# Performance work log

Hardware: AMD Instinct MI355X
Metric: run time of the kernel (lower is better)

Reference implementation:

```python
import jax, jax.numpy as jnp
import numpy as np

DIM = 1024
N_HEAD = 32
N_GROUP = 8
HEAD_DIM = DIM // N_HEAD  # 32
KV_DIM = N_GROUP * HEAD_DIM  # 256
BS, SEQ = 2, 2048


def setup_inputs() -> dict:
    key = jax.random.key(0)
    k1, k2, k3, k4 = jax.random.split(key, 4)
    x = jax.random.normal(k1, (BS, SEQ, DIM), dtype=jnp.float32)
    # nn.Linear weights, scaled like torch default init (~1/sqrt(fan_in))
    s = 1.0 / np.sqrt(DIM)
    wq = jax.random.normal(k2, (DIM, DIM), dtype=jnp.float32) * s
    wk = jax.random.normal(k3, (KV_DIM, DIM), dtype=jnp.float32) * s
    wv = jax.random.normal(k4, (KV_DIM, DIM), dtype=jnp.float32) * s
    return {"x": x, "wq": wq, "wk": wk, "wv": wv}


def reference(x, wq, wk, wv):
    bs, seq, _ = x.shape
    hpg = N_HEAD // N_GROUP  # heads per group
    # projections (torch Linear: x @ W.T)
    q = (x @ wq.T).reshape(bs, seq, N_GROUP, hpg, HEAD_DIM)
    k = (x @ wk.T).reshape(bs, seq, N_GROUP, HEAD_DIM)
    v = (x @ wv.T).reshape(bs, seq, N_GROUP, HEAD_DIM)
    # grouped attention: each KV group is shared by hpg query heads
    # (identical math to the expand/reshape in the torch source, no KV duplication)
    # NOTE: original applies NO 1/sqrt(head_dim) scaling and no mask.
    scores = jnp.einsum('bqgmd,bkgd->bgmqk', q, k)  # [bs, G, hpg, seq, seq]
    probs = jax.nn.softmax(scores, axis=-1)
    out = jnp.einsum('bgmqk,bkgd->bqgmd', probs, v)  # [bs, seq, G, hpg, hd]
    return out.reshape(bs, seq, N_HEAD * HEAD_DIM)
```

## Files before the change

### kernel.cpp

```cpp
#include <hip/hip_runtime.h>
#include <hip/hip_bf16.h>

#define BS   2
#define SEQ  2048
#define DIM  1024
#define HD   32
#define G    8
#define HPG  4
#define KVD  256
#define NTOT (DIM + 2*KVD)
#define NT2  (SEQ / 256)

typedef __attribute__((ext_vector_type(8))) _Float16 f16x8;
typedef __attribute__((ext_vector_type(4))) float f32x4;

__device__ __forceinline__ unsigned short f2h(float f) {
    _Float16 h = (_Float16)f;
    return __builtin_bit_cast(unsigned short, h);
}

__device__ __forceinline__ float fexp2(float x) { return __builtin_amdgcn_exp2f(x); }

#define GLDS(src, dst) __builtin_amdgcn_global_load_lds( \
    (const __attribute__((address_space(1))) unsigned int*)(src), \
    (__attribute__((address_space(3))) unsigned int*)(dst), 16, 0, 0)

#define NX4 1048576
__global__ __launch_bounds__(256) void cvt_all(const float* __restrict__ x,
                                               const float* __restrict__ wq,
                                               const float* __restrict__ wk,
                                               const float* __restrict__ wv,
                                               unsigned short* __restrict__ xb,
                                               unsigned short* __restrict__ wb) {
    int i = blockIdx.x * 256 + threadIdx.x;
    const float* src;
    unsigned short* dstb;
    int off, dsto;
    if (i < NX4) {
        src = x; off = i; dstb = xb; dsto = i;
    } else {
        int j = i - NX4;
        dstb = wb; dsto = j;
        if (j < 262144)      { src = wq; off = j; }
        else if (j < 327680) { src = wk; off = j - 262144; }
        else                 { src = wv; off = j - 327680; }
    }
    float4 v = reinterpret_cast<const float4*>(src)[off];
    ushort4 o;
    o.x = f2h(v.x); o.y = f2h(v.y); o.z = f2h(v.z); o.w = f2h(v.w);
    reinterpret_cast<ushort4*>(dstb)[dsto] = o;
}

__global__ __launch_bounds__(256) void qkv_gemm(const unsigned short* __restrict__ xb,
                                                const unsigned short* __restrict__ wb,
                                                unsigned short* __restrict__ qb,
                                                unsigned short* __restrict__ kb,
                                                unsigned short* __restrict__ vtb) {
    __shared__ unsigned short As[2][128 * 64];
    __shared__ unsigned short Bs[2][64 * 64];

    int tid  = threadIdx.x;
    int lane = tid & 63;
    int w    = tid >> 6;
    int m0   = blockIdx.y * 128;
    int n0   = blockIdx.x * 64;
    int lr = lane & 15, lq = lane >> 4;
    int wr = w >> 1, wc = w & 1;

    int srow = tid >> 3;
    int sg   = (tid & 7) ^ (srow & 7);
    const unsigned short* srcA = xb + (size_t)(m0 + srow) * DIM + sg * 8;
    const unsigned short* srcB = wb + (size_t)(n0 + srow) * DIM + sg * 8;

    #define GSTAGE(kt, buf) do { \
        GLDS(srcA + (kt),            &As[buf][tid * 8]); \
        GLDS(srcA + (kt) + 32 * DIM, &As[buf][(tid + 256) * 8]); \
        GLDS(srcA + (kt) + 64 * DIM, &As[buf][(tid + 512) * 8]); \
        GLDS(srcA + (kt) + 96 * DIM, &As[buf][(tid + 768) * 8]); \
        GLDS(srcB + (kt),            &Bs[buf][tid * 8]); \
        GLDS(srcB + (kt) + 32 * DIM, &Bs[buf][(tid + 256) * 8]); \
    } while (0)

    GSTAGE(0, 0);

    f32x4 acc[4][2] = {};
    int swz = lr & 7;

    for (int i = 0; i < 16; i++) {
        asm volatile("s_waitcnt vmcnt(0)" ::: "memory");
        __builtin_amdgcn_s_barrier();
        if (i + 1 < 16) GSTAGE((i + 1) * 64, (i + 1) & 1);

        const unsigned short* Ac = &As[i & 1][0];
        const unsigned short* Bc = &Bs[i & 1][0];

        #pragma unroll
        for (int ks = 0; ks < 2; ks++) {
            int c = ks * 4 + lq;
            f16x8 a[4], bfr[2];
            #pragma unroll
            for (int mi = 0; mi < 4; mi++) {
                int row = wr * 64 + mi * 16 + lr;
                a[mi] = *reinterpret_cast<const f16x8*>(Ac + row * 64 + (c ^ swz) * 8);
            }
            #pragma unroll
            for (int nf = 0; nf < 2; nf++) {
                int row = wc * 32 + nf * 16 + lr;
                bfr[nf] = *reinterpret_cast<const f16x8*>(Bc + row * 64 + (c ^ swz) * 8);
            }
            #pragma unroll
            for (int mi = 0; mi < 4; mi++)
                #pragma unroll
                for (int nf = 0; nf < 2; nf++)
                    acc[mi][nf] = __builtin_amdgcn_mfma_f32_16x16x32_f16(a[mi], bfr[nf], acc[mi][nf], 0, 0, 0);
        }
    }

    #pragma unroll
    for (int mi = 0; mi < 4; mi++) {
        #pragma unroll
        for (int nf = 0; nf < 2; nf++) {
            int col = n0 + wc * 32 + nf * 16 + lr;
            #pragma unroll
            for (int r = 0; r < 4; r++) {
                int row = m0 + wr * 64 + mi * 16 + lq * 4 + r;
                unsigned short v = f2h(acc[mi][nf][r]);
                if (col < DIM) {
                    qb[row * DIM + col] = v;
                } else if (col < DIM + KVD) {
                    kb[row * KVD + (col - DIM)] = v;
                } else {
                    int b = row >> 11, s = row & 2047;
                    int ps = (s & ~31) + ((s >> 2) & 3) * 8 + ((s >> 4) & 1) * 4 + (s & 3);
                    vtb[(b * KVD + (col - DIM - KVD)) * SEQ + ps] = v;
                }
            }
        }
    }
    #undef GSTAGE
}

__global__ __launch_bounds__(512) void gqa_attn(const unsigned short* __restrict__ qb,
                                                const unsigned short* __restrict__ kb,
                                                const unsigned short* __restrict__ vtb,
                                                float* __restrict__ out) {
    __shared__ unsigned short Ks[2][256 * 32];
    __shared__ unsigned short Vs[2][32 * 256];

    int tid  = threadIdx.x;
    int lane = tid & 63;
    int w    = tid >> 6;
    int head = w & 3;
    int qs   = (w >> 2) * 32;
    int bi   = blockIdx.x;
    int p  = bi & 15;
    int b  = p >> 3;
    int g  = p & 7;
    int qt = bi >> 4;
    int q0 = qt * 64;
    int lr = lane & 15, lq = lane >> 4;

    const unsigned short* kbase = kb + b * SEQ * KVD + g * HD;
    const unsigned short* vbase = vtb + (b * KVD + g * HD) * SEQ;

    int kr = tid >> 2;
    int swzK = (tid & 3) ^ ((kr >> 1) & 3);
    const unsigned short* srcK = kbase + kr * KVD + swzK * 8;
    int vr = tid >> 5;
    int swzV = (tid & 31) ^ (vr & 7);
    const unsigned short* srcV = vbase + vr * SEQ + swzV * 8;

    #define STAGE(tile, buf) do { \
        GLDS(srcK + (size_t)(tile) * 256 * KVD,             &Ks[buf][tid * 8]); \
        GLDS(srcK + (size_t)(tile) * 256 * KVD + 128 * KVD, &Ks[buf][(tid + 512) * 8]); \
        GLDS(srcV + (size_t)(tile) * 256,                   &Vs[buf][tid * 8]); \
        GLDS(srcV + (size_t)(tile) * 256 + 16 * SEQ,        &Vs[buf][(tid + 512) * 8]); \
    } while (0)

    STAGE(0, 0);

    f16x8 qf[2];
    #pragma unroll
    for (int t = 0; t < 2; t++) {
        qf[t] = *reinterpret_cast<const f16x8*>(
            qb + (b * SEQ + q0 + qs + t * 16 + lr) * DIM + (g * HPG + head) * HD + lq * 8);
        qf[t] = qf[t] * (_Float16)1.44269504f;
    }

    _Float16 one16 = (_Float16)1.0f;
    f16x8 ones = {one16, one16, one16, one16, one16, one16, one16, one16};

    f32x4 O[2][2] = {};
    f32x4 Lacc[2] = {};
    float m[2] = {0.f, 0.f};

    int koff = lr * 32 + ((lq ^ ((lr >> 1) & 3)) * 8);
    int vswz = lr & 7;

    for (int i = 0; i < NT2; i++) {
        asm volatile("s_waitcnt vmcnt(0)" ::: "memory");
        __builtin_amdgcn_s_barrier();
        if (i + 1 < NT2) STAGE(i + 1, (i + 1) & 1);

        const unsigned short* Kc = &Ks[i & 1][0];
        const unsigned short* Vc = &Vs[i & 1][0];

        #pragma unroll
        for (int h = 0; h < 2; h++) {
            const unsigned short* Kh = Kc + h * (128 * 32);
            const unsigned short* Vh = Vc + h * 128;

            f16x8 kf[8];
            #pragma unroll
            for (int kk = 0; kk < 8; kk++)
                kf[kk] = *reinterpret_cast<const f16x8*>(Kh + kk * 512 + koff);

            f16x8 vf[2][4];
            #pragma unroll
            for (int half = 0; half < 2; half++)
                #pragma unroll
                for (int kk2 = 0; kk2 < 4; kk2++)
                    vf[half][kk2] = *reinterpret_cast<const f16x8*>(
                        Vh + (half * 16 + lr) * 256 + (((kk2 * 4 + lq) ^ vswz) * 8));

            #pragma unroll
            for (int t = 0; t < 2; t++) {
                f32x4 zb = {-m[t], -m[t], -m[t], -m[t]};
                f32x4 s[8];
                __builtin_amdgcn_s_setprio(1);
                #pragma unroll
                for (int kk = 0; kk < 8; kk++)
                    s[kk] = __builtin_amdgcn_mfma_f32_16x16x32_f16(kf[kk], qf[t], zb, 0, 0, 0);
                __builtin_amdgcn_s_setprio(0);

                float tm = -1e30f;
                #pragma unroll
                for (int kk = 0; kk < 8; kk++)
                    tm = fmaxf(tm, fmaxf(fmaxf(s[kk][0], s[kk][1]), fmaxf(s[kk][2], s[kk][3])));

                if (!__all(tm <= 8.f)) {
                    float tw = fmaxf(tm, __shfl_xor(tm, 16, 64));
                    tw = fmaxf(tw, __shfl_xor(tw, 32, 64));
                    float delta = fmaxf(tw, 0.f);
                    float scl = fexp2(-delta);
                    m[t] += delta;
                    O[t][0] *= scl;
                    O[t][1] *= scl;
                    Lacc[t] *= scl;
                    f32x4 dv = {delta, delta, delta, delta};
                    #pragma unroll
                    for (int kk = 0; kk < 8; kk++) s[kk] -= dv;
                }

                #pragma unroll
                for (int kk = 0; kk < 8; kk++) {
                    s[kk][0] = fexp2(s[kk][0]);
                    s[kk][1] = fexp2(s[kk][1]);
                    s[kk][2] = fexp2(s[kk][2]);
                    s[kk][3] = fexp2(s[kk][3]);
                }

                #pragma unroll
                for (int kk2 = 0; kk2 < 4; kk2++) {
                    int c0 = __builtin_bit_cast(int, __builtin_amdgcn_cvt_pkrtz(s[2*kk2][0],   s[2*kk2][1]));
                    int c1 = __builtin_bit_cast(int, __builtin_amdgcn_cvt_pkrtz(s[2*kk2][2],   s[2*kk2][3]));
                    int c2 = __builtin_bit_cast(int, __builtin_amdgcn_cvt_pkrtz(s[2*kk2+1][0], s[2*kk2+1][1]));
                    int c3 = __builtin_bit_cast(int, __builtin_amdgcn_cvt_pkrtz(s[2*kk2+1][2], s[2*kk2+1][3]));
                    int4 pvi = {c0, c1, c2, c3};
                    f16x8 pa = __builtin_bit_cast(f16x8, pvi);
                    __builtin_amdgcn_s_setprio(1);
                    O[t][0] = __builtin_amdgcn_mfma_f32_16x16x32_f16(vf[0][kk2], pa, O[t][0], 0, 0, 0);
                    O[t][1] = __builtin_amdgcn_mfma_f32_16x16x32_f16(vf[1][kk2], pa, O[t][1], 0, 0, 0);
                    Lacc[t] = __builtin_amdgcn_mfma_f32_16x16x32_f16(ones, pa, Lacc[t], 0, 0, 0);
                    __builtin_amdgcn_s_setprio(0);
                }
            }
        }
    }

    float* obase = out + (size_t)(b * SEQ) * DIM + (g * HPG + head) * HD;
    #pragma unroll
    for (int t = 0; t < 2; t++) {
        float inv = 1.0f / Lacc[t][0];
        size_t rowoff = (size_t)(q0 + qs + t * 16 + lr) * DIM;
        float4 o0 = {O[t][0][0] * inv, O[t][0][1] * inv, O[t][0][2] * inv, O[t][0][3] * inv};
        float4 o1 = {O[t][1][0] * inv, O[t][1][1] * inv, O[t][1][2] * inv, O[t][1][3] * inv};
        *reinterpret_cast<float4*>(obase + rowoff + lq * 4)      = o0;
        *reinterpret_cast<float4*>(obase + rowoff + 16 + lq * 4) = o1;
    }
    #undef STAGE
}

extern "C" void kernel_launch(void* const* d_in, const int* in_sizes, int n_in,
                              void* d_out, int out_size, void* d_ws, size_t ws_size,
                              hipStream_t stream) {
    const float* x  = (const float*)d_in[0];
    const float* wq = (const float*)d_in[1];
    const float* wk = (const float*)d_in[2];
    const float* wv = (const float*)d_in[3];
    float* out = (float*)d_out;

    unsigned short* ws  = (unsigned short*)d_ws;
    unsigned short* xb  = ws;
    unsigned short* wb  = xb + (size_t)BS * SEQ * DIM;
    unsigned short* qb  = wb + (size_t)NTOT * DIM;
    unsigned short* kb  = qb + (size_t)BS * SEQ * DIM;
    unsigned short* vtb = kb + (size_t)BS * SEQ * KVD;

    cvt_all<<<(NX4 + 393216) / 256, 256, 0, stream>>>(x, wq, wk, wv, xb, wb);

    qkv_gemm<<<dim3(NTOT / 64, BS * SEQ / 128), 256, 0, stream>>>(xb, wb, qb, kb, vtb);
    gqa_attn<<<BS * G * (SEQ / 64), 512, 0, stream>>>(qb, kb, vtb, out);
}
```

Before: 95.05 us.

## Halve attention query tile and KV stage size to double grid parallelism

The attention kernel now handles 32 query rows per block instead of 64, with each wave owning one 16-row query tile rather than two. The K/V tiles staged into LDS shrink from 256 to 128 keys per iteration, which halves LDS use. The grid doubles to 1024 blocks, aiming for more occupancy and better load balance across CUs. The cost is twice the K/V global and LDS traffic per query row, since each loaded K/V fragment is reused by only one query tile, plus more barriers per block.

```diff
diff --git a/kernel.cpp b/kernel.cpp
--- a/kernel.cpp
+++ b/kernel.cpp
@@ -9,7 +9,7 @@
 #define HPG  4
 #define KVD  256
 #define NTOT (DIM + 2*KVD)
-#define NT2  (SEQ / 256)
+#define NT   (SEQ / 128)
 
 typedef __attribute__((ext_vector_type(8))) _Float16 f16x8;
 typedef __attribute__((ext_vector_type(4))) float f32x4;
@@ -144,20 +144,20 @@
                                                 const unsigned short* __restrict__ kb,
                                                 const unsigned short* __restrict__ vtb,
                                                 float* __restrict__ out) {
-    __shared__ unsigned short Ks[2][256 * 32];
-    __shared__ unsigned short Vs[2][32 * 256];
+    __shared__ unsigned short Ks[2][128 * 32];
+    __shared__ unsigned short Vs[2][32 * 128];
 
     int tid  = threadIdx.x;
     int lane = tid & 63;
     int w    = tid >> 6;
     int head = w & 3;
-    int qs   = (w >> 2) * 32;
+    int qs   = (w >> 2) * 16;
     int bi   = blockIdx.x;
     int p  = bi & 15;
     int b  = p >> 3;
     int g  = p & 7;
     int qt = bi >> 4;
-    int q0 = qt * 64;
+    int q0 = qt * 32;
     int lr = lane & 15, lq = lane >> 4;
 
     const unsigned short* kbase = kb + b * SEQ * KVD + g * HD;
@@ -166,128 +166,109 @@
     int kr = tid >> 2;
     int swzK = (tid & 3) ^ ((kr >> 1) & 3);
     const unsigned short* srcK = kbase + kr * KVD + swzK * 8;
-    int vr = tid >> 5;
-    int swzV = (tid & 31) ^ (vr & 7);
+    int vr = tid >> 4;
+    int swzV = (tid & 15) ^ (vr & 7);
     const unsigned short* srcV = vbase + vr * SEQ + swzV * 8;
 
     #define STAGE(tile, buf) do { \
-        GLDS(srcK + (size_t)(tile) * 256 * KVD,             &Ks[buf][tid * 8]); \
-        GLDS(srcK + (size_t)(tile) * 256 * KVD + 128 * KVD, &Ks[buf][(tid + 512) * 8]); \
-        GLDS(srcV + (size_t)(tile) * 256,                   &Vs[buf][tid * 8]); \
-        GLDS(srcV + (size_t)(tile) * 256 + 16 * SEQ,        &Vs[buf][(tid + 512) * 8]); \
+        GLDS(srcK + (size_t)(tile) * 128 * KVD, &Ks[buf][tid * 8]); \
+        GLDS(srcV + (size_t)(tile) * 128,       &Vs[buf][tid * 8]); \
     } while (0)
 
     STAGE(0, 0);
 
-    f16x8 qf[2];
-    #pragma unroll
-    for (int t = 0; t < 2; t++) {
-        qf[t] = *reinterpret_cast<const f16x8*>(
-            qb + (b * SEQ + q0 + qs + t * 16 + lr) * DIM + (g * HPG + head) * HD + lq * 8);
-        qf[t] = qf[t] * (_Float16)1.44269504f;
-    }
+    f16x8 qf = *reinterpret_cast<const f16x8*>(
+        qb + (b * SEQ + q0 + qs + lr) * DIM + (g * HPG + head) * HD + lq * 8);
+    qf = qf * (_Float16)1.44269504f;
 
     _Float16 one16 = (_Float16)1.0f;
     f16x8 ones = {one16, one16, one16, one16, one16, one16, one16, one16};
 
-    f32x4 O[2][2] = {};
-    f32x4 Lacc[2] = {};
-    float m[2] = {0.f, 0.f};
+    f32x4 O0 = {}, O1 = {};
+    f32x4 Lacc = {};
+    float m = 0.f;
 
     int koff = lr * 32 + ((lq ^ ((lr >> 1) & 3)) * 8);
-    int vswz = lr & 7;
-
-    for (int i = 0; i < NT2; i++) {
+
+    for (int i = 0; i < NT; i++) {
         asm volatile("s_waitcnt vmcnt(0)" ::: "memory");
         __builtin_amdgcn_s_barrier();
-        if (i + 1 < NT2) STAGE(i + 1, (i + 1) & 1);
+        if (i + 1 < NT) STAGE(i + 1, (i + 1) & 1);
 
         const unsigned short* Kc = &Ks[i & 1][0];
         const unsigned short* Vc = &Vs[i & 1][0];
 
-        #pragma unroll
-        for (int h = 0; h < 2; h++) {
-            const unsigned short* Kh = Kc + h * (128 * 32);
-            const unsigned short* Vh = Vc + h * 128;
-
-            f16x8 kf[8];
-            #pragma unroll
-            for (int kk = 0; kk < 8; kk++)
-                kf[kk] = *reinterpret_cast<const f16x8*>(Kh + kk * 512 + koff);
-
-            f16x8 vf[2][4];
-            #pragma unroll
-            for (int half = 0; half < 2; half++)
-                #pragma unroll
-                for (int kk2 = 0; kk2 < 4; kk2++)
-                    vf[half][kk2] = *reinterpret_cast<const f16x8*>(
-                        Vh + (half * 16 + lr) * 256 + (((kk2 * 4 + lq) ^ vswz) * 8));
-
-            #pragma unroll
-            for (int t = 0; t < 2; t++) {
-                f32x4 zb = {-m[t], -m[t], -m[t], -m[t]};
-                f32x4 s[8];
-                __builtin_amdgcn_s_setprio(1);
-                #pragma unroll
-                for (int kk = 0; kk < 8; kk++)
-                    s[kk] = __builtin_amdgcn_mfma_f32_16x16x32_f16(kf[kk], qf[t], zb, 0, 0, 0);
-                __builtin_amdgcn_s_setprio(0);
-
-                float tm = -1e30f;
-                #pragma unroll
-                for (int kk = 0; kk < 8; kk++)
-                    tm = fmaxf(tm, fmaxf(fmaxf(s[kk][0], s[kk][1]), fmaxf(s[kk][2], s[kk][3])));
-
-                if (!__all(tm <= 8.f)) {
-                    float tw = fmaxf(tm, __shfl_xor(tm, 16, 64));
-                    tw = fmaxf(tw, __shfl_xor(tw, 32, 64));
-                    float delta = fmaxf(tw, 0.f);
-                    float scl = fexp2(-delta);
-                    m[t] += delta;
-                    O[t][0] *= scl;
-                    O[t][1] *= scl;
-                    Lacc[t] *= scl;
-                    f32x4 dv = {delta, delta, delta, delta};
-                    #pragma unroll
-                    for (int kk = 0; kk < 8; kk++) s[kk] -= dv;
-                }
-
-                #pragma unroll
-                for (int kk = 0; kk < 8; kk++) {
-                    s[kk][0] = fexp2(s[kk][0]);
-                    s[kk][1] = fexp2(s[kk][1]);
-                    s[kk][2] = fexp2(s[kk][2]);
-                    s[kk][3] = fexp2(s[kk][3]);
-                }
-
-                #pragma unroll
-                for (int kk2 = 0; kk2 < 4; kk2++) {
-                    int c0 = __builtin_bit_cast(int, __builtin_amdgcn_cvt_pkrtz(s[2*kk2][0],   s[2*kk2][1]));
-                    int c1 = __builtin_bit_cast(int, __builtin_amdgcn_cvt_pkrtz(s[2*kk2][2],   s[2*kk2][3]));
-                    int c2 = __builtin_bit_cast(int, __builtin_amdgcn_cvt_pkrtz(s[2*kk2+1][0], s[2*kk2+1][1]));
-                    int c3 = __builtin_bit_cast(int, __builtin_amdgcn_cvt_pkrtz(s[2*kk2+1][2], s[2*kk2+1][3]));
-                    int4 pvi = {c0, c1, c2, c3};
-                    f16x8 pa = __builtin_bit_cast(f16x8, pvi);
-                    __builtin_amdgcn_s_setprio(1);
-                    O[t][0] = __builtin_amdgcn_mfma_f32_16x16x32_f16(vf[0][kk2], pa, O[t][0], 0, 0, 0);
-                    O[t][1] = __builtin_amdgcn_mfma_f32_16x16x32_f16(vf[1][kk2], pa, O[t][1], 0, 0, 0);
-                    Lacc[t] = __builtin_amdgcn_mfma_f32_16x16x32_f16(ones, pa, Lacc[t], 0, 0, 0);
-                    __builtin_amdgcn_s_setprio(0);
-                }
-            }
+        f16x8 kf[8];
+        #pragma unroll
+        for (int kk = 0; kk < 8; kk++)
+            kf[kk] = *reinterpret_cast<const f16x8*>(Kc + kk * 512 + koff);
+
+        f16x8 vf[2][4];
+        #pragma unroll
+        for (int half = 0; half < 2; half++)
+            #pragma unroll
+            for (int kk2 = 0; kk2 < 4; kk2++)
+                vf[half][kk2] = *reinterpret_cast<const f16x8*>(
+                    Vc + half * 2048 + lr * 128 + (((kk2 * 4 + lq) ^ (lr & 7)) * 8));
+
+        f32x4 zb = {-m, -m, -m, -m};
+        f32x4 s[8];
+        __builtin_amdgcn_s_setprio(1);
+        #pragma unroll
+        for (int kk = 0; kk < 8; kk++)
+            s[kk] = __builtin_amdgcn_mfma_f32_16x16x32_f16(kf[kk], qf, zb, 0, 0, 0);
+        __builtin_amdgcn_s_setprio(0);
+
+        float tm = -1e30f;
+        #pragma unroll
+        for (int kk = 0; kk < 8; kk++)
+            tm = fmaxf(tm, fmaxf(fmaxf(s[kk][0], s[kk][1]), fmaxf(s[kk][2], s[kk][3])));
+
+        if (!__all(tm <= 8.f)) {
+            float tw = fmaxf(tm, __shfl_xor(tm, 16, 64));
+            tw = fmaxf(tw, __shfl_xor(tw, 32, 64));
+            float delta = fmaxf(tw, 0.f);
+            float scl = fexp2(-delta);
+            m += delta;
+            O0 *= scl;
+            O1 *= scl;
+            Lacc *= scl;
+            f32x4 dv = {delta, delta, delta, delta};
+            #pragma unroll
+            for (int kk = 0; kk < 8; kk++) s[kk] -= dv;
+        }
+
+        #pragma unroll
+        for (int kk = 0; kk < 8; kk++) {
+            s[kk][0] = fexp2(s[kk][0]);
+            s[kk][1] = fexp2(s[kk][1]);
+            s[kk][2] = fexp2(s[kk][2]);
+            s[kk][3] = fexp2(s[kk][3]);
+        }
+
+        #pragma unroll
+        for (int kk2 = 0; kk2 < 4; kk2++) {
+            int c0 = __builtin_bit_cast(int, __builtin_amdgcn_cvt_pkrtz(s[2*kk2][0],   s[2*kk2][1]));
+            int c1 = __builtin_bit_cast(int, __builtin_amdgcn_cvt_pkrtz(s[2*kk2][2],   s[2*kk2][3]));
+            int c2 = __builtin_bit_cast(int, __builtin_amdgcn_cvt_pkrtz(s[2*kk2+1][0], s[2*kk2+1][1]));
+            int c3 = __builtin_bit_cast(int, __builtin_amdgcn_cvt_pkrtz(s[2*kk2+1][2], s[2*kk2+1][3]));
+            int4 pvi = {c0, c1, c2, c3};
+            f16x8 pa = __builtin_bit_cast(f16x8, pvi);
+            __builtin_amdgcn_s_setprio(1);
+            O0   = __builtin_amdgcn_mfma_f32_16x16x32_f16(vf[0][kk2], pa, O0, 0, 0, 0);
+            O1   = __builtin_amdgcn_mfma_f32_16x16x32_f16(vf[1][kk2], pa, O1, 0, 0, 0);
+            Lacc = __builtin_amdgcn_mfma_f32_16x16x32_f16(ones, pa, Lacc, 0, 0, 0);
+            __builtin_amdgcn_s_setprio(0);
         }
     }
 
     float* obase = out + (size_t)(b * SEQ) * DIM + (g * HPG + head) * HD;
-    #pragma unroll
-    for (int t = 0; t < 2; t++) {
-        float inv = 1.0f / Lacc[t][0];
-        size_t rowoff = (size_t)(q0 + qs + t * 16 + lr) * DIM;
-        float4 o0 = {O[t][0][0] * inv, O[t][0][1] * inv, O[t][0][2] * inv, O[t][0][3] * inv};
-        float4 o1 = {O[t][1][0] * inv, O[t][1][1] * inv, O[t][1][2] * inv, O[t][1][3] * inv};
-        *reinterpret_cast<float4*>(obase + rowoff + lq * 4)      = o0;
-        *reinterpret_cast<float4*>(obase + rowoff + 16 + lq * 4) = o1;
-    }
+    float inv = 1.0f / Lacc[0];
+    size_t rowoff = (size_t)(q0 + qs + lr) * DIM;
+    float4 o0 = {O0[0] * inv, O0[1] * inv, O0[2] * inv, O0[3] * inv};
+    float4 o1 = {O1[0] * inv, O1[1] * inv, O1[2] * inv, O1[3] * inv};
+    *reinterpret_cast<float4*>(obase + rowoff + lq * 4)      = o0;
+    *reinterpret_cast<float4*>(obase + rowoff + 16 + lq * 4) = o1;
     #undef STAGE
 }
 
@@ -310,5 +291,5 @@
     cvt_all<<<(NX4 + 393216) / 256, 256, 0, stream>>>(x, wq, wk, wv, xb, wb);
 
     qkv_gemm<<<dim3(NTOT / 64, BS * SEQ / 128), 256, 0, stream>>>(xb, wb, qb, kb, vtb);
-    gqa_attn<<<BS * G * (SEQ / 64), 512, 0, stream>>>(qb, kb, vtb, out);
-}
+    gqa_attn<<<BS * G * (SEQ / 32), 512, 0, stream>>>(qb, kb, vtb, out);
+}
```

New measurement: 90.92 us. 4.3% less time.
